# Kernel tuning notes

Hardware: AMD Instinct MI355X
Metric: run time of the kernel (lower is better)

The kernel has to match this reference:

```python
import jax, jax.numpy as jnp
import numpy as np

B, C, H, W = 32, 64, 32, 32
N = H * W  # 1024 spatial positions


def setup_inputs() -> dict:
    key = jax.random.key(0)
    ks = jax.random.split(key, 7)
    s_c = 1.0 / np.sqrt(C)
    s_n = 1.0 / np.sqrt(N)
    return {
        "x": jax.random.normal(ks[0], (B, C, H, W), dtype=jnp.float32),
        "w_phi": jax.random.normal(ks[1], (C, C), dtype=jnp.float32) * s_c,
        "w_theta": jax.random.normal(ks[2], (C, C), dtype=jnp.float32) * s_c,
        "w_g": jax.random.normal(ks[3], (C, C), dtype=jnp.float32) * s_c,
        "w_mask": jax.random.normal(ks[4], (C, C), dtype=jnp.float32) * s_c,
        "w_mv": jax.random.normal(ks[5], (C, C), dtype=jnp.float32) * s_c,
        "w_mk": jax.random.normal(ks[6], (N, N), dtype=jnp.float32) * s_n,
    }


def reference(x, w_phi, w_theta, w_g, w_mask, w_mv, w_mk):
    b, c, h, w = x.shape
    n = h * w
    xf = x.reshape(b, c, n)  # [b, c, N]
    # 1x1 convs == channel GEMMs (weight layout [out, in])
    phi = jnp.einsum("oc,bcn->bon", w_phi, xf)      # [b, c, N]
    theta = jnp.einsum("oc,bcn->bno", w_theta, xf)  # [b, N, c]
    g = jnp.einsum("oc,bcn->bno", w_g, xf)          # [b, N, c]
    # mv: Linear(c, c) on last dim of g  (y = g @ W^T)
    g = jnp.einsum("bnc,dc->bnd", g, w_mv)
    # theta @ phi -> [b, N, N]
    att = jnp.einsum("bnc,bcm->bnm", theta, phi)
    # mk: Linear(N, N) on last dim
    att = jnp.einsum("bnm,km->bnk", att, w_mk)
    # softmax over dim=1 (rows of the NxN map)
    att = jax.nn.softmax(att, axis=1)
    # att @ g -> [b, N, c]
    out = jnp.einsum("bnm,bmc->bnc", att, g)
    out = out.transpose(0, 2, 1).reshape(b, c, h, w)
    mask = jnp.einsum("oc,bchw->bohw", w_mask, out)
    return mask + x
```

## Files before the change

kernel.cpp:

```cpp
#include <hip/hip_runtime.h>

#define BB 32
#define CC 64
#define NN 1024

typedef __attribute__((ext_vector_type(8))) short bf8;
typedef __attribute__((ext_vector_type(4))) float f4;
typedef __attribute__((ext_vector_type(4))) unsigned short us4;

__device__ __forceinline__ unsigned short f2bf(float f) {
    unsigned u = __float_as_uint(f);
    return (unsigned short)((u + 0x7fffu + ((u >> 16) & 1u)) >> 16);
}
__device__ __forceinline__ float bf2f(unsigned short u) {
    return __uint_as_float(((unsigned)u) << 16);
}

#define MFMA(a, b, c) __builtin_amdgcn_mfma_f32_16x16x32_bf16(a, b, c, 0, 0, 0)

#define GLDS(g, l)                                                              \
    __builtin_amdgcn_global_load_lds(                                           \
        (const __attribute__((address_space(1))) void*)(g),                     \
        (__attribute__((address_space(3))) void*)(l), 16, 0, 0)

__device__ __forceinline__ void swz512(int i, int& b, int& t0) {
    int gid = (i & 7) * 64 + (i >> 3);
    b = gid >> 4;
    t0 = (gid & 15) * 64;
}

__global__ void k0_prep(const float* __restrict__ w_mv, const float* __restrict__ w_g,
                        const float* __restrict__ w_theta, const float* __restrict__ w_phi,
                        const float* __restrict__ w_mask, const float* __restrict__ w_mk,
                        unsigned short* __restrict__ wcat_bf,
                        unsigned short* __restrict__ wmask_bf,
                        unsigned short* __restrict__ wmk_bf) {
    int tid = threadIdx.x;
    if (blockIdx.x < 1024) {
        int i = (blockIdx.x * 256 + tid) * 4;
        float4 v = *(const float4*)(w_mk + i);
        us4 r;
        r.x = f2bf(v.x); r.y = f2bf(v.y); r.z = f2bf(v.z); r.w = f2bf(v.w);
        *(us4*)(wmk_bf + i) = r;
    } else {
        int idx = (blockIdx.x - 1024) * 256 + tid;
        int d = idx >> 6, e = idx & 63;
        float acc = 0.f;
        for (int c = 0; c < 64; ++c) acc += w_mv[d * 64 + c] * w_g[c * 64 + e];
        wcat_bf[idx] = f2bf(w_theta[idx]);
        wcat_bf[4096 + idx] = f2bf(w_phi[idx]);
        wcat_bf[8192 + idx] = f2bf(acc);
        wmask_bf[idx] = f2bf(w_mask[idx]);
    }
}

__global__ __launch_bounds__(256, 4) void k1_channel(const float* __restrict__ x,
                                                     const unsigned short* __restrict__ wcat,
                                                     unsigned short* __restrict__ theta_nc,
                                                     unsigned short* __restrict__ phi_cm,
                                                     unsigned short* __restrict__ g2_cm) {
    __shared__ __align__(16) unsigned short xT[32][72];
    int b = blockIdx.y;
    int n0 = blockIdx.x * 32;
    int tid = threadIdx.x;
    int w = tid >> 6, lane = tid & 63, l16 = lane & 15, q = lane >> 4;
    size_t bo = (size_t)b * CC * NN;
#pragma unroll
    for (int i = 0; i < 2; ++i) {
        int f = i * 1024 + tid * 4;
        int c = f >> 5, n = f & 31;
        float4 v = *(const float4*)(x + bo + (size_t)c * NN + n0 + n);
        xT[n + 0][c] = f2bf(v.x);
        xT[n + 1][c] = f2bf(v.y);
        xT[n + 2][c] = f2bf(v.z);
        xT[n + 3][c] = f2bf(v.w);
    }
    __syncthreads();
    bf8 bF[2][2];
#pragma unroll
    for (int ct = 0; ct < 2; ++ct) {
        bF[ct][0] = *(const bf8*)&xT[ct * 16 + l16][q * 8];
        bF[ct][1] = *(const bf8*)&xT[ct * 16 + l16][32 + q * 8];
    }
#pragma unroll
    for (int rt = 0; rt < 3; ++rt) {
        int R = w * 48 + rt * 16;
        const unsigned short* wa = wcat + (R + l16) * 64 + q * 8;
        bf8 a0 = *(const bf8*)wa;
        bf8 a1 = *(const bf8*)(wa + 32);
        int which = R >> 6, rb = R & 63;
#pragma unroll
        for (int ct = 0; ct < 2; ++ct) {
            f4 acc = {0.f, 0.f, 0.f, 0.f};
            acc = MFMA(a0, bF[ct][0], acc);
            acc = MFMA(a1, bF[ct][1], acc);
            int n = n0 + ct * 16 + l16;
            if (which == 0) {
                us4 t;
                t.x = f2bf(acc[0]); t.y = f2bf(acc[1]);
                t.z = f2bf(acc[2]); t.w = f2bf(acc[3]);
                *(us4*)&theta_nc[bo + (size_t)n * 64 + rb + q * 4] = t;
            } else {
                unsigned short* dst = (which == 1 ? phi_cm : g2_cm) + bo;
#pragma unroll
                for (int r = 0; r < 4; ++r)
                    dst[(size_t)(rb + q * 4 + r) * NN + n] = f2bf(acc[r]);
            }
        }
    }
}

__global__ __launch_bounds__(512, 4) void k23_phi2_stats(
    const unsigned short* __restrict__ phi_cm,
    const unsigned short* __restrict__ wmk_bf,
    const unsigned short* __restrict__ theta_nc,
    unsigned short* __restrict__ phi2t,
    float* __restrict__ sinv) {
    __shared__ __align__(16) unsigned short bT[2][4096];
    __shared__ __align__(16) unsigned short pT[64][72];
    __shared__ float sred[8][32];
    int b, k0;
    swz512(blockIdx.x, b, k0);
    int tid = threadIdx.x;
    int w = tid >> 6, lane = tid & 63, l16 = lane & 15, q = lane >> 4;
    size_t bo = (size_t)b * CC * NN;
    int srow = w * 8 + (lane >> 3);
    int scol = ((lane & 7) ^ (lane >> 3)) * 8;

    int ks = w & 3, ch = w >> 2;
    const unsigned short* gsrc = phi_cm + bo + (size_t)srow * NN + scol;
    const unsigned short* arow = wmk_bf + (size_t)(k0 + ks * 16 + l16) * NN + q * 8;
    f4 acc[2];
    acc[0] = (f4){0.f, 0.f, 0.f, 0.f};
    acc[1] = (f4){0.f, 0.f, 0.f, 0.f};
    bf8 aC0 = *(const bf8*)(arow);
    bf8 aC1 = *(const bf8*)(arow + 32);
    GLDS(gsrc, &bT[0][w * 512]);
    __syncthreads();
#pragma unroll 2
    for (int mc = 0; mc < 16; ++mc) {
        const unsigned short* bTc = bT[mc & 1];
        bf8 aN0 = aC0, aN1 = aC1;
        if (mc < 15) {
            int mn = (mc + 1) * 64;
            aN0 = *(const bf8*)(arow + mn);
            aN1 = *(const bf8*)(arow + mn + 32);
            GLDS(gsrc + mn, &bT[(mc + 1) & 1][w * 512]);
            asm volatile("s_waitcnt vmcnt(3)" ::: "memory");
        } else {
            asm volatile("s_waitcnt vmcnt(0)" ::: "memory");
        }
        __builtin_amdgcn_s_barrier();
        __builtin_amdgcn_sched_barrier(0);
#pragma unroll
        for (int t = 0; t < 2; ++t) {
            int row = (ch * 2 + t) * 16 + l16;
            int sw = (row & 7) * 8;
            bf8 b0 = *(const bf8*)&bTc[row * 64 + ((q * 8) ^ sw)];
            bf8 b1 = *(const bf8*)&bTc[row * 64 + ((32 + q * 8) ^ sw)];
            acc[t] = MFMA(aC0, b0, acc[t]);
            acc[t] = MFMA(aC1, b1, acc[t]);
        }
        __builtin_amdgcn_s_barrier();
        __builtin_amdgcn_sched_barrier(0);
        aC0 = aN0;
        aC1 = aN1;
    }
    unsigned short* prow = phi2t + bo;
#pragma unroll
    for (int t = 0; t < 2; ++t) {
        int ccol = (ch * 2 + t) * 16 + l16;
#pragma unroll
        for (int r = 0; r < 4; ++r) {
            int krow = ks * 16 + q * 4 + r;
            unsigned short v = f2bf(acc[t][r]);
            pT[krow][ccol] = v;
            prow[(size_t)(k0 + krow) * 64 + ccol] = v;
        }
    }

    int rg = w & 3, th = w >> 2;
    const unsigned short* thsrc = theta_nc + bo + (size_t)srow * 64 + scol;
    GLDS(thsrc, &bT[0][w * 512]);
    __syncthreads();
    bf8 pF[2][2];
#pragma unroll
    for (int t = 0; t < 2; ++t)
#pragma unroll
        for (int kc = 0; kc < 2; ++kc)
            pF[t][kc] = *(const bf8*)&pT[(th * 2 + t) * 16 + l16][kc * 32 + q * 8];
    float s[2] = {0.f, 0.f};
#pragma unroll 2
    for (int nc = 0; nc < 16; ++nc) {
        const unsigned short* tTc = bT[nc & 1];
        if (nc < 15) {
            GLDS(thsrc + (nc + 1) * 4096, &bT[(nc + 1) & 1][w * 512]);
            asm volatile("s_waitcnt vmcnt(1)" ::: "memory");
        } else {
            asm volatile("s_waitcnt vmcnt(0)" ::: "memory");
        }
        __builtin_amdgcn_s_barrier();
        __builtin_amdgcn_sched_barrier(0);
        int r = rg * 16 + l16;
        int sw = (r & 7);
        bf8 a0 = *(const bf8*)&tTc[r * 64 + ((q ^ sw) * 8)];
        bf8 a1 = *(const bf8*)&tTc[r * 64 + (((4 + q) ^ sw) * 8)];
#pragma unroll
        for (int t = 0; t < 2; ++t) {
            f4 at = {0.f, 0.f, 0.f, 0.f};
            at = MFMA(a0, pF[t][0], at);
            at = MFMA(a1, pF[t][1], at);
            s[t] += __expf(at[0]) + __expf(at[1]) + __expf(at[2]) + __expf(at[3]);
        }
        __builtin_amdgcn_s_barrier();
        __builtin_amdgcn_sched_barrier(0);
    }
#pragma unroll
    for (int t = 0; t < 2; ++t) {
        s[t] += __shfl_xor(s[t], 16, 64);
        s[t] += __shfl_xor(s[t], 32, 64);
    }
    if (q == 0) {
        sred[w][l16] = s[0];
        sred[w][16 + l16] = s[1];
    }
    __syncthreads();
    if (tid < 64) {
        int th2 = tid >> 5, rem = tid & 31;
        float S = sred[th2 * 4 + 0][rem] + sred[th2 * 4 + 1][rem] +
                  sred[th2 * 4 + 2][rem] + sred[th2 * 4 + 3][rem];
        sinv[(size_t)b * NN + k0 + tid] = 1.f / S;
    }
}

__global__ __launch_bounds__(512, 4) void k4_out(const unsigned short* __restrict__ theta_nc,
                                                 const unsigned short* __restrict__ phi2t,
                                                 const unsigned short* __restrict__ g2_cm,
                                                 const float* __restrict__ sinv,
                                                 const unsigned short* __restrict__ wmask_bf,
                                                 const float* __restrict__ x,
                                                 float* __restrict__ out) {
    __shared__ __align__(16) unsigned short smem[23040];
    float* svs_l = (float*)(smem + 20992);
    int b, n0;
    swz512(blockIdx.x, b, n0);
    int tid = threadIdx.x;
    int w = tid >> 6, lane = tid & 63, l16 = lane & 15, q = lane >> 4;
    int ws = w & 3, ph = w >> 2;
    int nl = ws * 16 + l16;
    size_t bo = (size_t)b * CC * NN;
    int srow = w * 8 + (lane >> 3);
    int scol = ((lane & 7) ^ (lane >> 3)) * 8;
    const unsigned short* p2b = phi2t + bo;
    const unsigned short* g2b = g2_cm + bo;
    if (tid < 256) *(f4*)&svs_l[tid * 4] = *(const f4*)(sinv + (size_t)b * NN + tid * 4);
    bf8 thB[2];
#pragma unroll
    for (int kc = 0; kc < 2; ++kc)
        thB[kc] = *(const bf8*)(theta_nc + bo + (size_t)(n0 + nl) * 64 + kc * 32 + q * 8);
    f4 accO[4];
#pragma unroll
    for (int ct = 0; ct < 4; ++ct) accO[ct] = (f4){0.f, 0.f, 0.f, 0.f};
    GLDS(p2b + (size_t)srow * 64 + scol, smem + w * 512);
    GLDS(g2b + (size_t)srow * NN + scol, smem + 4096 + w * 512);
    __syncthreads();
#pragma unroll 2
    for (int mc = 0; mc < 16; ++mc) {
        unsigned short* aT = smem + (mc & 1) * 8192;
        unsigned short* gT = aT + 4096;
        if (mc < 15) {
            int mn = (mc + 1) * 64;
            unsigned short* aN = smem + ((mc + 1) & 1) * 8192;
            GLDS(p2b + (size_t)(mn + srow) * 64 + scol, aN + w * 512);
            GLDS(g2b + (size_t)srow * NN + mn + scol, aN + 4096 + w * 512);
            asm volatile("s_waitcnt vmcnt(2)" ::: "memory");
        } else {
            asm volatile("s_waitcnt vmcnt(0)" ::: "memory");
        }
        __builtin_amdgcn_s_barrier();
        __builtin_amdgcn_sched_barrier(0);
        int m0 = mc * 64;
        unsigned short* Pr = smem + 16384 + nl * 72 + ph * 32;
        int swz = (l16 & 7) * 8;
#pragma unroll
        for (int mrr = 0; mrr < 2; ++mrr) {
            int rowA = ph * 32 + mrr * 16 + l16;
            bf8 a0 = *(const bf8*)&aT[rowA * 64 + ((q * 8) ^ swz)];
            bf8 a1 = *(const bf8*)&aT[rowA * 64 + ((32 + q * 8) ^ swz)];
            f4 at = {0.f, 0.f, 0.f, 0.f};
            at = MFMA(a0, thB[0], at);
            at = MFMA(a1, thB[1], at);
            f4 sv = *(const f4*)&svs_l[m0 + ph * 32 + mrr * 16 + q * 4];
            us4 pk;
            pk.x = f2bf(__expf(at[0]) * sv[0]);
            pk.y = f2bf(__expf(at[1]) * sv[1]);
            pk.z = f2bf(__expf(at[2]) * sv[2]);
            pk.w = f2bf(__expf(at[3]) * sv[3]);
            *(us4*)&Pr[mrr * 16 + q * 4] = pk;
        }
        bf8 pF = *(const bf8*)&Pr[q * 8];
#pragma unroll
        for (int ct = 0; ct < 4; ++ct) {
            int rowG = ct * 16 + l16;
            bf8 g0 = *(const bf8*)&gT[rowG * 64 + (((ph * 32) + q * 8) ^ swz)];
            accO[ct] = MFMA(g0, pF, accO[ct]);
        }
        __builtin_amdgcn_s_barrier();
        __builtin_amdgcn_sched_barrier(0);
    }
    float* o_red = (float*)smem;
    unsigned short* o_lds = smem + 8704;
    if (ph == 1) {
#pragma unroll
        for (int ct = 0; ct < 4; ++ct)
#pragma unroll
            for (int r = 0; r < 4; ++r) o_red[(ct * 16 + q * 4 + r) * 68 + nl] = accO[ct][r];
    }
    __syncthreads();
    if (ph == 0) {
#pragma unroll
        for (int ct = 0; ct < 4; ++ct) {
            us4 ov;
            ov.x = f2bf(accO[ct][0] + o_red[(ct * 16 + q * 4 + 0) * 68 + nl]);
            ov.y = f2bf(accO[ct][1] + o_red[(ct * 16 + q * 4 + 1) * 68 + nl]);
            ov.z = f2bf(accO[ct][2] + o_red[(ct * 16 + q * 4 + 2) * 68 + nl]);
            ov.w = f2bf(accO[ct][3] + o_red[(ct * 16 + q * 4 + 3) * 68 + nl]);
            *(us4*)&o_lds[nl * 72 + ct * 16 + q * 4] = ov;
        }
    }
    __syncthreads();
    bf8 oB0 = *(const bf8*)&o_lds[nl * 72 + q * 8];
    bf8 oB1 = *(const bf8*)&o_lds[nl * 72 + 32 + q * 8];
#pragma unroll
    for (int t2 = 0; t2 < 2; ++t2) {
        int tr = ph * 2 + t2;
        const unsigned short* wa = wmask_bf + (tr * 16 + l16) * 64 + q * 8;
        bf8 w0 = *(const bf8*)wa;
        bf8 w1 = *(const bf8*)(wa + 32);
        f4 accF = {0.f, 0.f, 0.f, 0.f};
        accF = MFMA(w0, oB0, accF);
        accF = MFMA(w1, oB1, accF);
#pragma unroll
        for (int r = 0; r < 4; ++r) {
            size_t ix = bo + (size_t)(tr * 16 + q * 4 + r) * NN + n0 + nl;
            out[ix] = accF[r] + x[ix];
        }
    }
}

extern "C" void kernel_launch(void* const* d_in, const int* in_sizes, int n_in,
                              void* d_out, int out_size, void* d_ws, size_t ws_size,
                              hipStream_t stream) {
    const float* x       = (const float*)d_in[0];
    const float* w_phi   = (const float*)d_in[1];
    const float* w_theta = (const float*)d_in[2];
    const float* w_g     = (const float*)d_in[3];
    const float* w_mask  = (const float*)d_in[4];
    const float* w_mv    = (const float*)d_in[5];
    const float* w_mk    = (const float*)d_in[6];
    float* out = (float*)d_out;

    const size_t CN = (size_t)BB * CC * NN;
    char* p = (char*)d_ws;
    unsigned short* theta_nc = (unsigned short*)p; p += CN * 2;
    unsigned short* phi_cm = (unsigned short*)p;   p += CN * 2;
    unsigned short* g2_cm = (unsigned short*)p;    p += CN * 2;
    float* sinv = (float*)p;                       p += CN * 2;
    unsigned short* phi2t = (unsigned short*)p;    p += CN * 2;
    unsigned short* wmk_bf = (unsigned short*)p;   p += (size_t)NN * NN * 2;
    unsigned short* wcat_bf = (unsigned short*)p;  p += 192 * 64 * 2;
    unsigned short* wmask_bf = (unsigned short*)p; p += 4096 * 2;

    k0_prep<<<1040, 256, 0, stream>>>(w_mv, w_g, w_theta, w_phi, w_mask, w_mk,
                                      wcat_bf, wmask_bf, wmk_bf);
    k1_channel<<<dim3(32, BB), 256, 0, stream>>>(x, wcat_bf, theta_nc, phi_cm, g2_cm);
    k23_phi2_stats<<<512, 512, 0, stream>>>(phi_cm, wmk_bf, theta_nc, phi2t, sinv);
    k4_out<<<512, 512, 0, stream>>>(theta_nc, phi2t, g2_cm, sinv, wmask_bf, x, out);
}
```

Before: 131.7 us.

## Fuse all four kernels into one persistent kernel with grid barriers

Merges the weight-prep, channel-projection, phi2/softmax-stats and output kernels into a single 512-block kernel separated by atomic-counter grid barriers, with a memset to reset the counter. The aim is to remove the launch gaps and tail effects between the four kernels. The channel stage is re-tiled to 64 positions per block to match the new grid. This relies on all 512 blocks being co-resident; the spin barrier adds atomic traffic and has a bounded timeout, so correctness depends on occupancy.

Result: slower. 307.3 us (+133.4%).

```diff
diff --git a/kernel.cpp b/kernel.cpp
--- a/kernel.cpp
+++ b/kernel.cpp
@@ -29,77 +29,102 @@
     t0 = (gid & 15) * 64;
 }
 
-__global__ void k0_prep(const float* __restrict__ w_mv, const float* __restrict__ w_g,
-                        const float* __restrict__ w_theta, const float* __restrict__ w_phi,
-                        const float* __restrict__ w_mask, const float* __restrict__ w_mk,
-                        unsigned short* __restrict__ wcat_bf,
-                        unsigned short* __restrict__ wmask_bf,
-                        unsigned short* __restrict__ wmk_bf) {
-    int tid = threadIdx.x;
-    if (blockIdx.x < 1024) {
-        int i = (blockIdx.x * 256 + tid) * 4;
-        float4 v = *(const float4*)(w_mk + i);
+__device__ __forceinline__ void gbar(unsigned* bar, int nb) {
+    __syncthreads();
+    if (threadIdx.x == 0) {
+        __threadfence();
+        unsigned ticket = atomicAdd(bar, 1u);
+        unsigned target = (ticket / (unsigned)nb + 1u) * (unsigned)nb;
+        for (int i = 0; i < (1 << 20); ++i) {
+            if (atomicAdd(bar, 0u) >= target) break;
+            __builtin_amdgcn_s_sleep(2);
+        }
+        __threadfence();
+    }
+    __syncthreads();
+}
+
+__global__ __launch_bounds__(512, 4) void k_all(
+    const float* __restrict__ x, const float* __restrict__ w_phi,
+    const float* __restrict__ w_theta, const float* __restrict__ w_g,
+    const float* __restrict__ w_mask, const float* __restrict__ w_mv,
+    const float* __restrict__ w_mk,
+    unsigned short* __restrict__ theta_nc, unsigned short* __restrict__ phi_cm,
+    unsigned short* __restrict__ g2_cm, float* __restrict__ sinv,
+    unsigned short* __restrict__ phi2t, unsigned short* __restrict__ wmk_bf,
+    unsigned short* __restrict__ wcat_bf, unsigned short* __restrict__ wmask_bf,
+    unsigned* bar, float* __restrict__ out) {
+    __shared__ __align__(16) unsigned short smem[23040];
+    const int tid = threadIdx.x;
+    const int bid = blockIdx.x;
+    const int w = tid >> 6, lane = tid & 63, l16 = lane & 15, q = lane >> 4;
+    int b, t0;
+    swz512(bid, b, t0);
+    const size_t bo = (size_t)b * CC * NN;
+    const int srow = w * 8 + (lane >> 3);
+    const int scol = ((lane & 7) ^ (lane >> 3)) * 8;
+
+    {
+        int i4 = (bid * 512 + tid) * 4;
+        float4 v = *(const float4*)(w_mk + i4);
         us4 r;
         r.x = f2bf(v.x); r.y = f2bf(v.y); r.z = f2bf(v.z); r.w = f2bf(v.w);
-        *(us4*)(wmk_bf + i) = r;
-    } else {
-        int idx = (blockIdx.x - 1024) * 256 + tid;
-        int d = idx >> 6, e = idx & 63;
-        float acc = 0.f;
-        for (int c = 0; c < 64; ++c) acc += w_mv[d * 64 + c] * w_g[c * 64 + e];
-        wcat_bf[idx] = f2bf(w_theta[idx]);
-        wcat_bf[4096 + idx] = f2bf(w_phi[idx]);
-        wcat_bf[8192 + idx] = f2bf(acc);
-        wmask_bf[idx] = f2bf(w_mask[idx]);
-    }
-}
-
-__global__ __launch_bounds__(256, 4) void k1_channel(const float* __restrict__ x,
-                                                     const unsigned short* __restrict__ wcat,
-                                                     unsigned short* __restrict__ theta_nc,
-                                                     unsigned short* __restrict__ phi_cm,
-                                                     unsigned short* __restrict__ g2_cm) {
-    __shared__ __align__(16) unsigned short xT[32][72];
-    int b = blockIdx.y;
-    int n0 = blockIdx.x * 32;
-    int tid = threadIdx.x;
-    int w = tid >> 6, lane = tid & 63, l16 = lane & 15, q = lane >> 4;
-    size_t bo = (size_t)b * CC * NN;
-#pragma unroll
-    for (int i = 0; i < 2; ++i) {
-        int f = i * 1024 + tid * 4;
-        int c = f >> 5, n = f & 31;
-        float4 v = *(const float4*)(x + bo + (size_t)c * NN + n0 + n);
-        xT[n + 0][c] = f2bf(v.x);
-        xT[n + 1][c] = f2bf(v.y);
-        xT[n + 2][c] = f2bf(v.z);
-        xT[n + 3][c] = f2bf(v.w);
-    }
-    __syncthreads();
-    bf8 bF[2][2];
-#pragma unroll
-    for (int ct = 0; ct < 2; ++ct) {
-        bF[ct][0] = *(const bf8*)&xT[ct * 16 + l16][q * 8];
-        bF[ct][1] = *(const bf8*)&xT[ct * 16 + l16][32 + q * 8];
-    }
-#pragma unroll
-    for (int rt = 0; rt < 3; ++rt) {
-        int R = w * 48 + rt * 16;
-        const unsigned short* wa = wcat + (R + l16) * 64 + q * 8;
-        bf8 a0 = *(const bf8*)wa;
-        bf8 a1 = *(const bf8*)(wa + 32);
-        int which = R >> 6, rb = R & 63;
-#pragma unroll
-        for (int ct = 0; ct < 2; ++ct) {
+        *(us4*)(wmk_bf + i4) = r;
+        if (bid < 32) {
+            int idx = bid * 512 + tid;
+            if (idx < 4096) {
+                wcat_bf[idx] = f2bf(w_theta[idx]);
+            } else if (idx < 8192) {
+                wcat_bf[idx] = f2bf(w_phi[idx - 4096]);
+            } else if (idx < 12288) {
+                int s = idx - 8192, d = s >> 6, e = s & 63;
+                float acc = 0.f;
+                for (int c = 0; c < 64; ++c) acc += w_mv[d * 64 + c] * w_g[c * 64 + e];
+                wcat_bf[idx] = f2bf(acc);
+            } else {
+                wmask_bf[idx - 12288] = f2bf(w_mask[idx - 12288]);
+            }
+        }
+    }
+    gbar(bar, 512);
+
+    {
+        unsigned short* xT = smem;
+        int n0 = t0;
+#pragma unroll
+        for (int i = 0; i < 2; ++i) {
+            int idx = i * 512 + tid;
+            int c = idx >> 4, n4 = (idx & 15) * 4;
+            float4 v = *(const float4*)(x + bo + (size_t)c * NN + n0 + n4);
+            xT[(n4 + 0) * 72 + c] = f2bf(v.x);
+            xT[(n4 + 1) * 72 + c] = f2bf(v.y);
+            xT[(n4 + 2) * 72 + c] = f2bf(v.z);
+            xT[(n4 + 3) * 72 + c] = f2bf(v.w);
+        }
+        __syncthreads();
+        bf8 bF[4][2];
+#pragma unroll
+        for (int ct = 0; ct < 4; ++ct) {
+            bF[ct][0] = *(const bf8*)&xT[(ct * 16 + l16) * 72 + q * 8];
+            bF[ct][1] = *(const bf8*)&xT[(ct * 16 + l16) * 72 + 32 + q * 8];
+        }
+#pragma unroll
+        for (int i = 0; i < 6; ++i) {
+            int t = w * 6 + i;
+            int R = (t >> 2) * 16, ct = t & 3;
+            const unsigned short* wa = wcat_bf + (R + l16) * 64 + q * 8;
+            bf8 a0 = *(const bf8*)wa;
+            bf8 a1 = *(const bf8*)(wa + 32);
+            int which = R >> 6, rb = R & 63;
             f4 acc = {0.f, 0.f, 0.f, 0.f};
             acc = MFMA(a0, bF[ct][0], acc);
             acc = MFMA(a1, bF[ct][1], acc);
             int n = n0 + ct * 16 + l16;
             if (which == 0) {
-                us4 t;
-                t.x = f2bf(acc[0]); t.y = f2bf(acc[1]);
-                t.z = f2bf(acc[2]); t.w = f2bf(acc[3]);
-                *(us4*)&theta_nc[bo + (size_t)n * 64 + rb + q * 4] = t;
+                us4 tt;
+                tt.x = f2bf(acc[0]); tt.y = f2bf(acc[1]);
+                tt.z = f2bf(acc[2]); tt.w = f2bf(acc[3]);
+                *(us4*)&theta_nc[bo + (size_t)n * 64 + rb + q * 4] = tt;
             } else {
                 unsigned short* dst = (which == 1 ? phi_cm : g2_cm) + bo;
 #pragma unroll
@@ -108,242 +133,218 @@
             }
         }
     }
-}
-
-__global__ __launch_bounds__(512, 4) void k23_phi2_stats(
-    const unsigned short* __restrict__ phi_cm,
-    const unsigned short* __restrict__ wmk_bf,
-    const unsigned short* __restrict__ theta_nc,
-    unsigned short* __restrict__ phi2t,
-    float* __restrict__ sinv) {
-    __shared__ __align__(16) unsigned short bT[2][4096];
-    __shared__ __align__(16) unsigned short pT[64][72];
-    __shared__ float sred[8][32];
-    int b, k0;
-    swz512(blockIdx.x, b, k0);
-    int tid = threadIdx.x;
-    int w = tid >> 6, lane = tid & 63, l16 = lane & 15, q = lane >> 4;
-    size_t bo = (size_t)b * CC * NN;
-    int srow = w * 8 + (lane >> 3);
-    int scol = ((lane & 7) ^ (lane >> 3)) * 8;
-
-    int ks = w & 3, ch = w >> 2;
-    const unsigned short* gsrc = phi_cm + bo + (size_t)srow * NN + scol;
-    const unsigned short* arow = wmk_bf + (size_t)(k0 + ks * 16 + l16) * NN + q * 8;
-    f4 acc[2];
-    acc[0] = (f4){0.f, 0.f, 0.f, 0.f};
-    acc[1] = (f4){0.f, 0.f, 0.f, 0.f};
-    bf8 aC0 = *(const bf8*)(arow);
-    bf8 aC1 = *(const bf8*)(arow + 32);
-    GLDS(gsrc, &bT[0][w * 512]);
-    __syncthreads();
+    gbar(bar, 512);
+
+    {
+        int k0 = t0;
+        unsigned short* bT0 = smem;
+        unsigned short(*pT)[72] = (unsigned short(*)[72])(smem + 8192);
+        float(*sred)[32] = (float(*)[32])(void*)(smem + 12800);
+        int ks = w & 3, ch = w >> 2;
+        const unsigned short* gsrc = phi_cm + bo + (size_t)srow * NN + scol;
+        const unsigned short* arow = wmk_bf + (size_t)(k0 + ks * 16 + l16) * NN + q * 8;
+        f4 acc[2];
+        acc[0] = (f4){0.f, 0.f, 0.f, 0.f};
+        acc[1] = (f4){0.f, 0.f, 0.f, 0.f};
+        bf8 aC0 = *(const bf8*)(arow);
+        bf8 aC1 = *(const bf8*)(arow + 32);
+        GLDS(gsrc, bT0 + w * 512);
+        __syncthreads();
 #pragma unroll 2
-    for (int mc = 0; mc < 16; ++mc) {
-        const unsigned short* bTc = bT[mc & 1];
-        bf8 aN0 = aC0, aN1 = aC1;
-        if (mc < 15) {
-            int mn = (mc + 1) * 64;
-            aN0 = *(const bf8*)(arow + mn);
-            aN1 = *(const bf8*)(arow + mn + 32);
-            GLDS(gsrc + mn, &bT[(mc + 1) & 1][w * 512]);
-            asm volatile("s_waitcnt vmcnt(3)" ::: "memory");
-        } else {
-            asm volatile("s_waitcnt vmcnt(0)" ::: "memory");
-        }
-        __builtin_amdgcn_s_barrier();
-        __builtin_amdgcn_sched_barrier(0);
+        for (int mc = 0; mc < 16; ++mc) {
+            const unsigned short* bTc = bT0 + (mc & 1) * 4096;
+            bf8 aN0 = aC0, aN1 = aC1;
+            if (mc < 15) {
+                int mn = (mc + 1) * 64;
+                aN0 = *(const bf8*)(arow + mn);
+                aN1 = *(const bf8*)(arow + mn + 32);
+                GLDS(gsrc + mn, bT0 + ((mc + 1) & 1) * 4096 + w * 512);
+                asm volatile("s_waitcnt vmcnt(3)" ::: "memory");
+            } else {
+                asm volatile("s_waitcnt vmcnt(0)" ::: "memory");
+            }
+            __builtin_amdgcn_s_barrier();
+            __builtin_amdgcn_sched_barrier(0);
+#pragma unroll
+            for (int t = 0; t < 2; ++t) {
+                int row = (ch * 2 + t) * 16 + l16;
+                int sw = (row & 7) * 8;
+                bf8 b0 = *(const bf8*)&bTc[row * 64 + ((q * 8) ^ sw)];
+                bf8 b1 = *(const bf8*)&bTc[row * 64 + ((32 + q * 8) ^ sw)];
+                acc[t] = MFMA(aC0, b0, acc[t]);
+                acc[t] = MFMA(aC1, b1, acc[t]);
+            }
+            __builtin_amdgcn_s_barrier();
+            __builtin_amdgcn_sched_barrier(0);
+            aC0 = aN0;
+            aC1 = aN1;
+        }
+        unsigned short* prow = phi2t + bo;
 #pragma unroll
         for (int t = 0; t < 2; ++t) {
-            int row = (ch * 2 + t) * 16 + l16;
-            int sw = (row & 7) * 8;
-            bf8 b0 = *(const bf8*)&bTc[row * 64 + ((q * 8) ^ sw)];
-            bf8 b1 = *(const bf8*)&bTc[row * 64 + ((32 + q * 8) ^ sw)];
-            acc[t] = MFMA(aC0, b0, acc[t]);
-            acc[t] = MFMA(aC1, b1, acc[t]);
-        }
-        __builtin_amdgcn_s_barrier();
-        __builtin_amdgcn_sched_barrier(0);
-        aC0 = aN0;
-        aC1 = aN1;
-    }
-    unsigned short* prow = phi2t + bo;
-#pragma unroll
-    for (int t = 0; t < 2; ++t) {
-        int ccol = (ch * 2 + t) * 16 + l16;
-#pragma unroll
-        for (int r = 0; r < 4; ++r) {
-            int krow = ks * 16 + q * 4 + r;
-            unsigned short v = f2bf(acc[t][r]);
-            pT[krow][ccol] = v;
-            prow[(size_t)(k0 + krow) * 64 + ccol] = v;
-        }
-    }
-
-    int rg = w & 3, th = w >> 2;
-    const unsigned short* thsrc = theta_nc + bo + (size_t)srow * 64 + scol;
-    GLDS(thsrc, &bT[0][w * 512]);
-    __syncthreads();
-    bf8 pF[2][2];
-#pragma unroll
-    for (int t = 0; t < 2; ++t)
+            int ccol = (ch * 2 + t) * 16 + l16;
+#pragma unroll
+            for (int r = 0; r < 4; ++r) {
+                int krow = ks * 16 + q * 4 + r;
+                unsigned short v = f2bf(acc[t][r]);
+                pT[krow][ccol] = v;
+                prow[(size_t)(k0 + krow) * 64 + ccol] = v;
+            }
+        }
+        int rg = w & 3, th = w >> 2;
+        const unsigned short* thsrc = theta_nc + bo + (size_t)srow * 64 + scol;
+        GLDS(thsrc, bT0 + w * 512);
+        __syncthreads();
+        bf8 pF[2][2];
+#pragma unroll
+        for (int t = 0; t < 2; ++t)
+#pragma unroll
+            for (int kc = 0; kc < 2; ++kc)
+                pF[t][kc] = *(const bf8*)&pT[(th * 2 + t) * 16 + l16][kc * 32 + q * 8];
+        float s[2] = {0.f, 0.f};
+#pragma unroll 2
+        for (int nc = 0; nc < 16; ++nc) {
+            const unsigned short* tTc = bT0 + (nc & 1) * 4096;
+            if (nc < 15) {
+                GLDS(thsrc + (nc + 1) * 4096, bT0 + ((nc + 1) & 1) * 4096 + w * 512);
+                asm volatile("s_waitcnt vmcnt(1)" ::: "memory");
+            } else {
+                asm volatile("s_waitcnt vmcnt(0)" ::: "memory");
+            }
+            __builtin_amdgcn_s_barrier();
+            __builtin_amdgcn_sched_barrier(0);
+            int r = rg * 16 + l16;
+            int sw = (r & 7);
+            bf8 a0 = *(const bf8*)&tTc[r * 64 + ((q ^ sw) * 8)];
+            bf8 a1 = *(const bf8*)&tTc[r * 64 + (((4 + q) ^ sw) * 8)];
+#pragma unroll
+            for (int t = 0; t < 2; ++t) {
+                f4 at = {0.f, 0.f, 0.f, 0.f};
+                at = MFMA(a0, pF[t][0], at);
+                at = MFMA(a1, pF[t][1], at);
+                s[t] += __expf(at[0]) + __expf(at[1]) + __expf(at[2]) + __expf(at[3]);
+            }
+            __builtin_amdgcn_s_barrier();
+            __builtin_amdgcn_sched_barrier(0);
+        }
+#pragma unroll
+        for (int t = 0; t < 2; ++t) {
+            s[t] += __shfl_xor(s[t], 16, 64);
+            s[t] += __shfl_xor(s[t], 32, 64);
+        }
+        if (q == 0) {
+            sred[w][l16] = s[0];
+            sred[w][16 + l16] = s[1];
+        }
+        __syncthreads();
+        if (tid < 64) {
+            int th2 = tid >> 5, rem = tid & 31;
+            float S = sred[th2 * 4 + 0][rem] + sred[th2 * 4 + 1][rem] +
+                      sred[th2 * 4 + 2][rem] + sred[th2 * 4 + 3][rem];
+            sinv[(size_t)b * NN + k0 + tid] = 1.f / S;
+        }
+    }
+    gbar(bar, 512);
+
+    {
+        int n0 = t0;
+        float* svs_l = (float*)(smem + 20992);
+        int ws = w & 3, ph = w >> 2;
+        int nl = ws * 16 + l16;
+        const unsigned short* p2b = phi2t + bo;
+        const unsigned short* g2b = g2_cm + bo;
+        if (tid < 256) *(f4*)&svs_l[tid * 4] = *(const f4*)(sinv + (size_t)b * NN + tid * 4);
+        bf8 thB[2];
 #pragma unroll
         for (int kc = 0; kc < 2; ++kc)
-            pF[t][kc] = *(const bf8*)&pT[(th * 2 + t) * 16 + l16][kc * 32 + q * 8];
-    float s[2] = {0.f, 0.f};
+            thB[kc] = *(const bf8*)(theta_nc + bo + (size_t)(n0 + nl) * 64 + kc * 32 + q * 8);
+        f4 accO[4];
+#pragma unroll
+        for (int ct = 0; ct < 4; ++ct) accO[ct] = (f4){0.f, 0.f, 0.f, 0.f};
+        GLDS(p2b + (size_t)srow * 64 + scol, smem + w * 512);
+        GLDS(g2b + (size_t)srow * NN + scol, smem + 4096 + w * 512);
+        __syncthreads();
 #pragma unroll 2
-    for (int nc = 0; nc < 16; ++nc) {
-        const unsigned short* tTc = bT[nc & 1];
-        if (nc < 15) {
-            GLDS(thsrc + (nc + 1) * 4096, &bT[(nc + 1) & 1][w * 512]);
-            asm volatile("s_waitcnt vmcnt(1)" ::: "memory");
-        } else {
-            asm volatile("s_waitcnt vmcnt(0)" ::: "memory");
-        }
-        __builtin_amdgcn_s_barrier();
-        __builtin_amdgcn_sched_barrier(0);
-        int r = rg * 16 + l16;
-        int sw = (r & 7);
-        bf8 a0 = *(const bf8*)&tTc[r * 64 + ((q ^ sw) * 8)];
-        bf8 a1 = *(const bf8*)&tTc[r * 64 + (((4 + q) ^ sw) * 8)];
-#pragma unroll
-        for (int t = 0; t < 2; ++t) {
-            f4 at = {0.f, 0.f, 0.f, 0.f};
-            at = MFMA(a0, pF[t][0], at);
-            at = MFMA(a1, pF[t][1], at);
-            s[t] += __expf(at[0]) + __expf(at[1]) + __expf(at[2]) + __expf(at[3]);
-        }
-        __builtin_amdgcn_s_barrier();
-        __builtin_amdgcn_sched_barrier(0);
-    }
-#pragma unroll
-    for (int t = 0; t < 2; ++t) {
-        s[t] += __shfl_xor(s[t], 16, 64);
-        s[t] += __shfl_xor(s[t], 32, 64);
-    }
-    if (q == 0) {
-        sred[w][l16] = s[0];
-        sred[w][16 + l16] = s[1];
-    }
-    __syncthreads();
-    if (tid < 64) {
-        int th2 = tid >> 5, rem = tid & 31;
-        float S = sred[th2 * 4 + 0][rem] + sred[th2 * 4 + 1][rem] +
-                  sred[th2 * 4 + 2][rem] + sred[th2 * 4 + 3][rem];
-        sinv[(size_t)b * NN + k0 + tid] = 1.f / S;
-    }
-}
-
-__global__ __launch_bounds__(512, 4) void k4_out(const unsigned short* __restrict__ theta_nc,
-                                                 const unsigned short* __restrict__ phi2t,
-                                                 const unsigned short* __restrict__ g2_cm,
-                                                 const float* __restrict__ sinv,
-                                                 const unsigned short* __restrict__ wmask_bf,
-                                                 const float* __restrict__ x,
-                                                 float* __restrict__ out) {
-    __shared__ __align__(16) unsigned short smem[23040];
-    float* svs_l = (float*)(smem + 20992);
-    int b, n0;
-    swz512(blockIdx.x, b, n0);
-    int tid = threadIdx.x;
-    int w = tid >> 6, lane = tid & 63, l16 = lane & 15, q = lane >> 4;
-    int ws = w & 3, ph = w >> 2;
-    int nl = ws * 16 + l16;
-    size_t bo = (size_t)b * CC * NN;
-    int srow = w * 8 + (lane >> 3);
-    int scol = ((lane & 7) ^ (lane >> 3)) * 8;
-    const unsigned short* p2b = phi2t + bo;
-    const unsigned short* g2b = g2_cm + bo;
-    if (tid < 256) *(f4*)&svs_l[tid * 4] = *(const f4*)(sinv + (size_t)b * NN + tid * 4);
-    bf8 thB[2];
-#pragma unroll
-    for (int kc = 0; kc < 2; ++kc)
-        thB[kc] = *(const bf8*)(theta_nc + bo + (size_t)(n0 + nl) * 64 + kc * 32 + q * 8);
-    f4 accO[4];
-#pragma unroll
-    for (int ct = 0; ct < 4; ++ct) accO[ct] = (f4){0.f, 0.f, 0.f, 0.f};
-    GLDS(p2b + (size_t)srow * 64 + scol, smem + w * 512);
-    GLDS(g2b + (size_t)srow * NN + scol, smem + 4096 + w * 512);
-    __syncthreads();
-#pragma unroll 2
-    for (int mc = 0; mc < 16; ++mc) {
-        unsigned short* aT = smem + (mc & 1) * 8192;
-        unsigned short* gT = aT + 4096;
-        if (mc < 15) {
-            int mn = (mc + 1) * 64;
-            unsigned short* aN = smem + ((mc + 1) & 1) * 8192;
-            GLDS(p2b + (size_t)(mn + srow) * 64 + scol, aN + w * 512);
-            GLDS(g2b + (size_t)srow * NN + mn + scol, aN + 4096 + w * 512);
-            asm volatile("s_waitcnt vmcnt(2)" ::: "memory");
-        } else {
-            asm volatile("s_waitcnt vmcnt(0)" ::: "memory");
-        }
-        __builtin_amdgcn_s_barrier();
-        __builtin_amdgcn_sched_barrier(0);
-        int m0 = mc * 64;
-        unsigned short* Pr = smem + 16384 + nl * 72 + ph * 32;
-        int swz = (l16 & 7) * 8;
-#pragma unroll
-        for (int mrr = 0; mrr < 2; ++mrr) {
-            int rowA = ph * 32 + mrr * 16 + l16;
-            bf8 a0 = *(const bf8*)&aT[rowA * 64 + ((q * 8) ^ swz)];
-            bf8 a1 = *(const bf8*)&aT[rowA * 64 + ((32 + q * 8) ^ swz)];
-            f4 at = {0.f, 0.f, 0.f, 0.f};
-            at = MFMA(a0, thB[0], at);
-            at = MFMA(a1, thB[1], at);
-            f4 sv = *(const f4*)&svs_l[m0 + ph * 32 + mrr * 16 + q * 4];
-            us4 pk;
-            pk.x = f2bf(__expf(at[0]) * sv[0]);
-            pk.y = f2bf(__expf(at[1]) * sv[1]);
-            pk.z = f2bf(__expf(at[2]) * sv[2]);
-            pk.w = f2bf(__expf(at[3]) * sv[3]);
-            *(us4*)&Pr[mrr * 16 + q * 4] = pk;
-        }
-        bf8 pF = *(const bf8*)&Pr[q * 8];
-#pragma unroll
-        for (int ct = 0; ct < 4; ++ct) {
-            int rowG = ct * 16 + l16;
-            bf8 g0 = *(const bf8*)&gT[rowG * 64 + (((ph * 32) + q * 8) ^ swz)];
-            accO[ct] = MFMA(g0, pF, accO[ct]);
-        }
-        __builtin_amdgcn_s_barrier();
-        __builtin_amdgcn_sched_barrier(0);
-    }
-    float* o_red = (float*)smem;
-    unsigned short* o_lds = smem + 8704;
-    if (ph == 1) {
-#pragma unroll
-        for (int ct = 0; ct < 4; ++ct)
-#pragma unroll
-            for (int r = 0; r < 4; ++r) o_red[(ct * 16 + q * 4 + r) * 68 + nl] = accO[ct][r];
-    }
-    __syncthreads();
-    if (ph == 0) {
-#pragma unroll
-        for (int ct = 0; ct < 4; ++ct) {
-            us4 ov;
-            ov.x = f2bf(accO[ct][0] + o_red[(ct * 16 + q * 4 + 0) * 68 + nl]);
-            ov.y = f2bf(accO[ct][1] + o_red[(ct * 16 + q * 4 + 1) * 68 + nl]);
-            ov.z = f2bf(accO[ct][2] + o_red[(ct * 16 + q * 4 + 2) * 68 + nl]);
-            ov.w = f2bf(accO[ct][3] + o_red[(ct * 16 + q * 4 + 3) * 68 + nl]);
-            *(us4*)&o_lds[nl * 72 + ct * 16 + q * 4] = ov;
-        }
-    }
-    __syncthreads();
-    bf8 oB0 = *(const bf8*)&o_lds[nl * 72 + q * 8];
-    bf8 oB1 = *(const bf8*)&o_lds[nl * 72 + 32 + q * 8];
-#pragma unroll
-    for (int t2 = 0; t2 < 2; ++t2) {
-        int tr = ph * 2 + t2;
-        const unsigned short* wa = wmask_bf + (tr * 16 + l16) * 64 + q * 8;
-        bf8 w0 = *(const bf8*)wa;
-        bf8 w1 = *(const bf8*)(wa + 32);
-        f4 accF = {0.f, 0.f, 0.f, 0.f};
-        accF = MFMA(w0, oB0, accF);
-        accF = MFMA(w1, oB1, accF);
-#pragma unroll
-        for (int r = 0; r < 4; ++r) {
-            size_t ix = bo + (size_t)(tr * 16 + q * 4 + r) * NN + n0 + nl;
-            out[ix] = accF[r] + x[ix];
+        for (int mc = 0; mc < 16; ++mc) {
+            unsigned short* aT = smem + (mc & 1) * 8192;
+            unsigned short* gT = aT + 4096;
+            if (mc < 15) {
+                int mn = (mc + 1) * 64;
+                unsigned short* aN = smem + ((mc + 1) & 1) * 8192;
+                GLDS(p2b + (size_t)(mn + srow) * 64 + scol, aN + w * 512);
+                GLDS(g2b + (size_t)srow * NN + mn + scol, aN + 4096 + w * 512);
+                asm volatile("s_waitcnt vmcnt(2)" ::: "memory");
+            } else {
+                asm volatile("s_waitcnt vmcnt(0)" ::: "memory");
+            }
+            __builtin_amdgcn_s_barrier();
+            __builtin_amdgcn_sched_barrier(0);
+            int m0 = mc * 64;
+            unsigned short* Pr = smem + 16384 + nl * 72 + ph * 32;
+            int swz = (l16 & 7) * 8;
+#pragma unroll
+            for (int mrr = 0; mrr < 2; ++mrr) {
+                int rowA = ph * 32 + mrr * 16 + l16;
+                bf8 a0 = *(const bf8*)&aT[rowA * 64 + ((q * 8) ^ swz)];
+                bf8 a1 = *(const bf8*)&aT[rowA * 64 + ((32 + q * 8) ^ swz)];
+                f4 at = {0.f, 0.f, 0.f, 0.f};
+                at = MFMA(a0, thB[0], at);
+                at = MFMA(a1, thB[1], at);
+                f4 sv = *(const f4*)&svs_l[m0 + ph * 32 + mrr * 16 + q * 4];
+                us4 pk;
+                pk.x = f2bf(__expf(at[0]) * sv[0]);
+                pk.y = f2bf(__expf(at[1]) * sv[1]);
+                pk.z = f2bf(__expf(at[2]) * sv[2]);
+                pk.w = f2bf(__expf(at[3]) * sv[3]);
+                *(us4*)&Pr[mrr * 16 + q * 4] = pk;
+            }
+            bf8 pF = *(const bf8*)&Pr[q * 8];
+#pragma unroll
+            for (int ct = 0; ct < 4; ++ct) {
+                int rowG = ct * 16 + l16;
+                bf8 g0 = *(const bf8*)&gT[rowG * 64 + (((ph * 32) + q * 8) ^ swz)];
+                accO[ct] = MFMA(g0, pF, accO[ct]);
+            }
+            __builtin_amdgcn_s_barrier();
+            __builtin_amdgcn_sched_barrier(0);
+        }
+        float* o_red = (float*)smem;
+        unsigned short* o_lds = smem + 8704;
+        if (ph == 1) {
+#pragma unroll
+            for (int ct = 0; ct < 4; ++ct)
+#pragma unroll
+                for (int r = 0; r < 4; ++r) o_red[(ct * 16 + q * 4 + r) * 68 + nl] = accO[ct][r];
+        }
+        __syncthreads();
+        if (ph == 0) {
+#pragma unroll
+            for (int ct = 0; ct < 4; ++ct) {
+                us4 ov;
+                ov.x = f2bf(accO[ct][0] + o_red[(ct * 16 + q * 4 + 0) * 68 + nl]);
+                ov.y = f2bf(accO[ct][1] + o_red[(ct * 16 + q * 4 + 1) * 68 + nl]);
+                ov.z = f2bf(accO[ct][2] + o_red[(ct * 16 + q * 4 + 2) * 68 + nl]);
+                ov.w = f2bf(accO[ct][3] + o_red[(ct * 16 + q * 4 + 3) * 68 + nl]);
+                *(us4*)&o_lds[nl * 72 + ct * 16 + q * 4] = ov;
+            }
+        }
+        __syncthreads();
+        bf8 oB0 = *(const bf8*)&o_lds[nl * 72 + q * 8];
+        bf8 oB1 = *(const bf8*)&o_lds[nl * 72 + 32 + q * 8];
+#pragma unroll
+        for (int t2 = 0; t2 < 2; ++t2) {
+            int tr = ph * 2 + t2;
+            const unsigned short* wa = wmask_bf + (tr * 16 + l16) * 64 + q * 8;
+            bf8 w0 = *(const bf8*)wa;
+            bf8 w1 = *(const bf8*)(wa + 32);
+            f4 accF = {0.f, 0.f, 0.f, 0.f};
+            accF = MFMA(w0, oB0, accF);
+            accF = MFMA(w1, oB1, accF);
+#pragma unroll
+            for (int r = 0; r < 4; ++r) {
+                size_t ix = bo + (size_t)(tr * 16 + q * 4 + r) * NN + n0 + nl;
+                out[ix] = accF[r] + x[ix];
+            }
         }
     }
 }
@@ -370,10 +371,10 @@
     unsigned short* wmk_bf = (unsigned short*)p;   p += (size_t)NN * NN * 2;
     unsigned short* wcat_bf = (unsigned short*)p;  p += 192 * 64 * 2;
     unsigned short* wmask_bf = (unsigned short*)p; p += 4096 * 2;
-
-    k0_prep<<<1040, 256, 0, stream>>>(w_mv, w_g, w_theta, w_phi, w_mask, w_mk,
-                                      wcat_bf, wmask_bf, wmk_bf);
-    k1_channel<<<dim3(32, BB), 256, 0, stream>>>(x, wcat_bf, theta_nc, phi_cm, g2_cm);
-    k23_phi2_stats<<<512, 512, 0, stream>>>(phi_cm, wmk_bf, theta_nc, phi2t, sinv);
-    k4_out<<<512, 512, 0, stream>>>(theta_nc, phi2t, g2_cm, sinv, wmask_bf, x, out);
-}
+    unsigned* bar = (unsigned*)p;                  p += 256;
+
+    hipMemsetAsync((void*)bar, 0, 256, stream);
+    k_all<<<512, 512, 0, stream>>>(x, w_phi, w_theta, w_g, w_mask, w_mv, w_mk,
+                                   theta_nc, phi_cm, g2_cm, sinv, phi2t,
+                                   wmk_bf, wcat_bf, wmask_bf, bar, out);
+}
```
